# Performance work log

Measured on AMD Instinct MI355X. Metric: run time of the kernel, lower is better.

The kernel has to match this reference:

```python
import jax, jax.numpy as jnp
import numpy as np

EMBED_DIM = 768
NUM_HEADS = 12
HEAD_DIM = EMBED_DIM // NUM_HEADS


def setup_inputs() -> dict:
    key = jax.random.key(0)
    kx, kq, kk, kv, ko = jax.random.split(key, 5)
    B, S, D = 2, 2048, EMBED_DIM
    scale = 1.0 / np.sqrt(D)
    x = jax.random.normal(kx, (B, S, D), dtype=jnp.float32)
    # nn.Linear weight is [out, in]; y = x @ W.T. Store as [in, out] for y = x @ W.
    Wq = jax.random.normal(kq, (D, D), dtype=jnp.float32) * scale
    Wk = jax.random.normal(kk, (D, D), dtype=jnp.float32) * scale
    Wv = jax.random.normal(kv, (D, D), dtype=jnp.float32) * scale
    Wo = jax.random.normal(ko, (D, D), dtype=jnp.float32) * scale
    return {"x": x, "Wq": Wq, "Wk": Wk, "Wv": Wv, "Wo": Wo}


def reference(x, Wq, Wk, Wv, Wo):
    B, S, D = x.shape
    H, Hd = NUM_HEADS, HEAD_DIM
    # projections -> [B, H, S, Hd]
    q = (x @ Wq).reshape(B, S, H, Hd).transpose(0, 2, 1, 3)
    k = (x @ Wk).reshape(B, S, H, Hd).transpose(0, 2, 1, 3)
    v = (x @ Wv).reshape(B, S, H, Hd).transpose(0, 2, 1, 3)
    # scores [B, H, S, S], scaled by sqrt(head_dim)
    scores = jnp.einsum('bhqd,bhkd->bhqk', q, k) / jnp.sqrt(jnp.float32(Hd))
    attn = jax.nn.softmax(scores, axis=-1)
    out = jnp.einsum('bhqk,bhkd->bhqd', attn, v)  # [B, H, S, Hd]
    out = out.transpose(0, 2, 1, 3).reshape(B, S, D)
    return out @ Wo
```

## Files before the change

### kernel.cpp

```cpp
#include <hip/hip_runtime.h>
#include <hip/hip_bf16.h>
#include <cstdint>
#include <math.h>

#define DIM   768

typedef __bf16 bf16x8 __attribute__((ext_vector_type(8)));
typedef __bf16 bf16x2 __attribute__((ext_vector_type(2)));
typedef float f32x4 __attribute__((ext_vector_type(4)));
typedef unsigned short u16x8 __attribute__((ext_vector_type(8)));
typedef unsigned short u16x4 __attribute__((ext_vector_type(4)));

static __device__ __forceinline__ unsigned short f2bf(float f) {
  union { float f; unsigned u; } a; a.f = f;
  unsigned u = a.u;
  u += 0x7fffu + ((u >> 16) & 1u);
  return (unsigned short)(u >> 16);
}
static __device__ __forceinline__ unsigned pk2(float a, float b) {
  union { bf16x2 v; unsigned u; } x;
  x.v[0] = (__bf16)a; x.v[1] = (__bf16)b;
  return x.u;
}

static __device__ __forceinline__ f32x4 mfma16(bf16x8 a, bf16x8 b, f32x4 c) {
  return __builtin_amdgcn_mfma_f32_16x16x32_bf16(a, b, c, 0, 0, 0);
}

static __device__ __forceinline__ bf16x8 ld_bf8(const unsigned short* p) {
  return *reinterpret_cast<const bf16x8*>(p);
}

static __device__ __forceinline__ void gload_lds16(const void* g, void* l) {
  __builtin_amdgcn_global_load_lds(
      (const __attribute__((address_space(1))) void*)g,
      (__attribute__((address_space(3))) void*)l, 16, 0, 0);
}

#define EXP2 __builtin_amdgcn_exp2f

__global__ void k_cvt_x(const float* __restrict__ x, unsigned short* __restrict__ xb) {
  int i = (blockIdx.x * 256 + threadIdx.x) * 4;
  float4 v = *reinterpret_cast<const float4*>(x + i);
  u16x4 o;
  o[0] = f2bf(v.x); o[1] = f2bf(v.y); o[2] = f2bf(v.z); o[3] = f2bf(v.w);
  *reinterpret_cast<u16x4*>(xb + i) = o;
}

__global__ void k_tw(const float* __restrict__ Wq, const float* __restrict__ Wk,
                     const float* __restrict__ Wv, const float* __restrict__ Wo,
                     unsigned short* __restrict__ wqkvt, unsigned short* __restrict__ wot) {
  __shared__ unsigned short tile[64][68];
  const int wsel = blockIdx.z;
  const float* W = wsel == 0 ? Wq : wsel == 1 ? Wk : wsel == 2 ? Wv : Wo;
  const int n0 = blockIdx.x * 64, k0 = blockIdx.y * 64;
  const int t = threadIdx.x;
  const int kr = t >> 4, nc = (t & 15) * 4;
  for (int p = 0; p < 4; ++p) {
    int kk = kr + p * 16;
    float4 v = *reinterpret_cast<const float4*>(W + (size_t)(k0 + kk) * DIM + n0 + nc);
    tile[kk][nc]     = f2bf(v.x);
    tile[kk][nc + 1] = f2bf(v.y);
    tile[kk][nc + 2] = f2bf(v.z);
    tile[kk][nc + 3] = f2bf(v.w);
  }
  __syncthreads();
  const int nr = t >> 3, kc = (t & 7) * 8;
  for (int p = 0; p < 2; ++p) {
    int nn = nr + p * 32;
    u16x8 o;
    for (int j = 0; j < 8; ++j) o[j] = tile[kc + j][nn];
    unsigned short* dst = (wsel < 3)
        ? wqkvt + (size_t)(wsel * DIM + n0 + nn) * DIM + k0 + kc
        : wot + (size_t)(n0 + nn) * DIM + k0 + kc;
    *reinterpret_cast<u16x8*>(dst) = o;
  }
}

template <int EPI>
__global__ __launch_bounds__(256, 2) void k_gemm(
    const unsigned short* __restrict__ A, const unsigned short* __restrict__ Bt,
    unsigned short* __restrict__ qws, unsigned short* __restrict__ kws,
    unsigned short* __restrict__ vtws, float* __restrict__ out) {
  __shared__ alignas(16) unsigned short lA[128 * 64];
  __shared__ alignas(16) unsigned short lB[128 * 64];
  const int t = threadIdx.x;
  const int lane = t & 63, w = t >> 6;
  const int wr = w >> 1, wc = w & 1;
  const int r15 = lane & 15, rhi = lane >> 4;
  const int m0 = blockIdx.x * 128, n0 = blockIdx.y * 128;

  f32x4 acc[4][4] = {};

  for (int kt = 0; kt < 12; ++kt) {
    const int k0 = kt * 64;
    for (int i = 0; i < 4; ++i) {
      int f = i * 256 + t;
      int row = f >> 3;
      int cb = (f & 7) ^ (row & 7);
      gload_lds16(A + (size_t)(m0 + row) * DIM + k0 + cb * 8, (char*)lA + f * 16);
      gload_lds16(Bt + (size_t)(n0 + row) * DIM + k0 + cb * 8, (char*)lB + f * 16);
    }
    __syncthreads();
    for (int kk = 0; kk < 2; ++kk) {
      bf16x8 av[4], bv[4];
      for (int m = 0; m < 4; ++m) {
        int row = wr * 64 + m * 16 + r15;
        int cb = (kk * 4 + rhi) ^ (row & 7);
        av[m] = ld_bf8(lA + row * 64 + cb * 8);
      }
      for (int n = 0; n < 4; ++n) {
        int row = wc * 64 + n * 16 + r15;
        int cb = (kk * 4 + rhi) ^ (row & 7);
        bv[n] = ld_bf8(lB + row * 64 + cb * 8);
      }
      for (int m = 0; m < 4; ++m)
        for (int n = 0; n < 4; ++n)
          acc[m][n] = mfma16(av[m], bv[n], acc[m][n]);
    }
    __syncthreads();
  }

  for (int m = 0; m < 4; ++m) {
    for (int n = 0; n < 4; ++n) {
      for (int r = 0; r < 4; ++r) {
        int row = m0 + wr * 64 + m * 16 + rhi * 4 + r;
        int col = n0 + wc * 64 + n * 16 + r15;
        float v = acc[m][n][r];
        if (EPI == 0) {
          int wsel = col >= 1536 ? 2 : (col >= 768 ? 1 : 0);
          int c = col - wsel * 768;
          int h = c >> 6, d = c & 63;
          int b = row >> 11, s = row & 2047;
          size_t bh = (size_t)b * 12 + h;
          unsigned short bb = f2bf(v);
          if (wsel == 0)      qws[(bh * 2048 + s) * 64 + d] = bb;
          else if (wsel == 1) kws[(bh * 2048 + s) * 64 + d] = bb;
          else                vtws[(bh * 64 + d) * 2048 + s] = bb;
        } else {
          out[(size_t)row * DIM + col] = v;
        }
      }
    }
  }
}

__global__ __launch_bounds__(256) void k_attn(
    const unsigned short* __restrict__ qws, const unsigned short* __restrict__ kws,
    const unsigned short* __restrict__ vtws, unsigned short* __restrict__ ows) {
  __shared__ alignas(16) unsigned short lK[64 * 64];
  __shared__ alignas(16) unsigned short lV[64 * 64];
  __shared__ alignas(16) unsigned short lP[4][16 * 72];
  const int t = threadIdx.x;
  const int lane = t & 63, w = t >> 6;
  const int r15 = lane & 15, rhi = lane >> 4;
  const int bh = blockIdx.x;
  const int q0 = blockIdx.y * 64 + w * 16;
  const float SC = 0.18033688011112042f;

  const size_t qrow = ((size_t)bh * 2048 + q0 + r15) * 64;
  bf16x8 qa0 = ld_bf8(qws + qrow + rhi * 8);
  bf16x8 qa1 = ld_bf8(qws + qrow + 32 + rhi * 8);

  f32x4 oaccT[4] = {};
  float mrun = -INFINITY, lrun = 0.f;

  unsigned short* P = &lP[w][0];
  unsigned* Pw = (unsigned*)P;

  for (int kv = 0; kv < 2048; kv += 64) {
    for (int i = 0; i < 2; ++i) {
      int f = i * 256 + t;
      int row = f >> 3;
      int cb = (f & 7) ^ (row & 7);
      gload_lds16(kws + ((size_t)bh * 2048 + kv + row) * 64 + cb * 8, (char*)lK + f * 16);
      gload_lds16(vtws + ((size_t)bh * 64 + row) * 2048 + kv + cb * 8, (char*)lV + f * 16);
    }
    __syncthreads();

    f32x4 sT[4];
#pragma unroll
    for (int n = 0; n < 4; ++n) {
      int row = n * 16 + r15;
      bf16x8 b0 = ld_bf8(lK + row * 64 + ((rhi) ^ (row & 7)) * 8);
      bf16x8 b1 = ld_bf8(lK + row * 64 + ((4 + rhi) ^ (row & 7)) * 8);
      f32x4 z = {0.f, 0.f, 0.f, 0.f};
      z = mfma16(b0, qa0, z);
      z = mfma16(b1, qa1, z);
      sT[n] = z;
    }

    float mp = sT[0][0];
#pragma unroll
    for (int n = 0; n < 4; ++n)
      for (int r = 0; r < 4; ++r) mp = fmaxf(mp, sT[n][r]);
    mp = fmaxf(mp, __shfl_xor(mp, 16));
    mp = fmaxf(mp, __shfl_xor(mp, 32));
    float mps = mp * SC;

    if (!__all(mps <= mrun + 8.0f)) {
      float mn = fmaxf(mrun, mps);
      float fac = EXP2(mrun - mn);
      mrun = mn;
      lrun *= fac;
#pragma unroll
      for (int nd = 0; nd < 4; ++nd)
        for (int r = 0; r < 4; ++r) oaccT[nd][r] *= fac;
    }

    float p[4][4];
    float rs = 0.f;
#pragma unroll
    for (int n = 0; n < 4; ++n)
      for (int r = 0; r < 4; ++r) {
        p[n][r] = EXP2(fmaf(sT[n][r], SC, -mrun));
        rs += p[n][r];
      }
    rs += __shfl_xor(rs, 16);
    rs += __shfl_xor(rs, 32);
    lrun += rs;

#pragma unroll
    for (int n = 0; n < 4; ++n) {
      int kj = n * 16 + rhi * 4;
      Pw[r15 * 36 + (kj >> 1)]     = pk2(p[n][0], p[n][1]);
      Pw[r15 * 36 + (kj >> 1) + 1] = pk2(p[n][2], p[n][3]);
    }

    bf16x8 pa0 = ld_bf8(P + r15 * 72 + rhi * 8);
    bf16x8 pa1 = ld_bf8(P + r15 * 72 + 32 + rhi * 8);
#pragma unroll
    for (int nd = 0; nd < 4; ++nd) {
      int row = nd * 16 + r15;
      bf16x8 v0 = ld_bf8(lV + row * 64 + ((rhi) ^ (row & 7)) * 8);
      bf16x8 v1 = ld_bf8(lV + row * 64 + ((4 + rhi) ^ (row & 7)) * 8);
      oaccT[nd] = mfma16(v0, pa0, oaccT[nd]);
      oaccT[nd] = mfma16(v1, pa1, oaccT[nd]);
    }
    __syncthreads();
  }

  const int b = bh / 12, h = bh % 12;
  float inv = 1.0f / lrun;
  unsigned short* dst = ows + ((size_t)b * 2048 + q0 + r15) * DIM + h * 64;
#pragma unroll
  for (int nd = 0; nd < 4; ++nd) {
    int d = nd * 16 + rhi * 4;
    *(unsigned*)(dst + d)     = pk2(oaccT[nd][0] * inv, oaccT[nd][1] * inv);
    *(unsigned*)(dst + d + 2) = pk2(oaccT[nd][2] * inv, oaccT[nd][3] * inv);
  }
}

extern "C" void kernel_launch(void* const* d_in, const int* in_sizes, int n_in,
                              void* d_out, int out_size, void* d_ws, size_t ws_size,
                              hipStream_t stream) {
  (void)in_sizes; (void)n_in; (void)out_size;
  const float* x  = (const float*)d_in[0];
  const float* Wq = (const float*)d_in[1];
  const float* Wk = (const float*)d_in[2];
  const float* Wv = (const float*)d_in[3];
  const float* Wo = (const float*)d_in[4];
  float* out = (float*)d_out;

  char* ws = (char*)d_ws;
  unsigned short* xb    = (unsigned short*)(ws);
  unsigned short* wqkvt = (unsigned short*)(ws + 6291456);
  unsigned short* wot   = (unsigned short*)(ws + 9830400);
  unsigned short* qws   = (unsigned short*)(ws + 11010048);
  unsigned short* kws   = (unsigned short*)(ws + 17301504);
  unsigned short* vtws  = (unsigned short*)(ws + 23592960);
  unsigned short* ows   = (unsigned short*)(ws + 29884416);
  if (ws_size < 36175872u) return;

  k_cvt_x<<<3072, 256, 0, stream>>>(x, xb);
  k_tw<<<dim3(12, 12, 4), 256, 0, stream>>>(Wq, Wk, Wv, Wo, wqkvt, wot);
  k_gemm<0><<<dim3(32, 18), 256, 0, stream>>>(xb, wqkvt, qws, kws, vtws, nullptr);
  k_attn<<<dim3(24, 32), 256, 0, stream>>>(qws, kws, vtws, ows);
  k_gemm<1><<<dim3(32, 6), 256, 0, stream>>>(ows, wot, nullptr, nullptr, nullptr, out);
}
```

Before: 170.2 us.

## Double-buffer K/V tiles in attention kernel to overlap loads with compute

Splits the K and V LDS tiles into two buffers and issues the direct-to-LDS global loads for the next KV block before computing on the current one. One of the two barriers per iteration is dropped, and global load address calculation is hoisted out of the loop. The aim is to hide global memory latency behind the MFMA and softmax work. In exchange it doubles the K/V shared memory, which may lower occupancy, and it relies on the async loads having completed by the single barrier.

```diff
diff --git a/kernel.cpp b/kernel.cpp
--- a/kernel.cpp
+++ b/kernel.cpp
@@ -148,8 +148,8 @@
 __global__ __launch_bounds__(256) void k_attn(
     const unsigned short* __restrict__ qws, const unsigned short* __restrict__ kws,
     const unsigned short* __restrict__ vtws, unsigned short* __restrict__ ows) {
-  __shared__ alignas(16) unsigned short lK[64 * 64];
-  __shared__ alignas(16) unsigned short lV[64 * 64];
+  __shared__ alignas(16) unsigned short lK[2][64 * 64];
+  __shared__ alignas(16) unsigned short lV[2][64 * 64];
   __shared__ alignas(16) unsigned short lP[4][16 * 72];
   const int t = threadIdx.x;
   const int lane = t & 63, w = t >> 6;
@@ -158,6 +158,14 @@
   const int q0 = blockIdx.y * 64 + w * 16;
   const float SC = 0.18033688011112042f;
 
+  const int f0 = t, f1 = 256 + t;
+  const int row0 = f0 >> 3, row1 = f1 >> 3;
+  const int cb0 = (f0 & 7) ^ (row0 & 7), cb1 = (f1 & 7) ^ (row1 & 7);
+  const unsigned short* kg0 = kws + ((size_t)bh * 2048 + row0) * 64 + cb0 * 8;
+  const unsigned short* kg1 = kws + ((size_t)bh * 2048 + row1) * 64 + cb1 * 8;
+  const unsigned short* vg0 = vtws + ((size_t)bh * 64 + row0) * 2048 + cb0 * 8;
+  const unsigned short* vg1 = vtws + ((size_t)bh * 64 + row1) * 2048 + cb1 * 8;
+
   const size_t qrow = ((size_t)bh * 2048 + q0 + r15) * 64;
   bf16x8 qa0 = ld_bf8(qws + qrow + rhi * 8);
   bf16x8 qa1 = ld_bf8(qws + qrow + 32 + rhi * 8);
@@ -168,22 +176,29 @@
   unsigned short* P = &lP[w][0];
   unsigned* Pw = (unsigned*)P;
 
+#define STAGE(buf, kv) do { \
+    gload_lds16(kg0 + (size_t)(kv) * 64, (char*)lK[buf] + f0 * 16); \
+    gload_lds16(kg1 + (size_t)(kv) * 64, (char*)lK[buf] + f1 * 16); \
+    gload_lds16(vg0 + (kv),              (char*)lV[buf] + f0 * 16); \
+    gload_lds16(vg1 + (kv),              (char*)lV[buf] + f1 * 16); \
+  } while (0)
+
+  STAGE(0, 0);
+  __syncthreads();
+
+  int cur = 0;
   for (int kv = 0; kv < 2048; kv += 64) {
-    for (int i = 0; i < 2; ++i) {
-      int f = i * 256 + t;
-      int row = f >> 3;
-      int cb = (f & 7) ^ (row & 7);
-      gload_lds16(kws + ((size_t)bh * 2048 + kv + row) * 64 + cb * 8, (char*)lK + f * 16);
-      gload_lds16(vtws + ((size_t)bh * 64 + row) * 2048 + kv + cb * 8, (char*)lV + f * 16);
-    }
-    __syncthreads();
+    if (kv + 64 < 2048) STAGE(cur ^ 1, kv + 64);
+
+    const unsigned short* Kc = lK[cur];
+    const unsigned short* Vc = lV[cur];
 
     f32x4 sT[4];
 #pragma unroll
     for (int n = 0; n < 4; ++n) {
       int row = n * 16 + r15;
-      bf16x8 b0 = ld_bf8(lK + row * 64 + ((rhi) ^ (row & 7)) * 8);
-      bf16x8 b1 = ld_bf8(lK + row * 64 + ((4 + rhi) ^ (row & 7)) * 8);
+      bf16x8 b0 = ld_bf8(Kc + row * 64 + ((rhi) ^ (row & 7)) * 8);
+      bf16x8 b1 = ld_bf8(Kc + row * 64 + ((4 + rhi) ^ (row & 7)) * 8);
       f32x4 z = {0.f, 0.f, 0.f, 0.f};
       z = mfma16(b0, qa0, z);
       z = mfma16(b1, qa1, z);
@@ -232,13 +247,16 @@
 #pragma unroll
     for (int nd = 0; nd < 4; ++nd) {
       int row = nd * 16 + r15;
-      bf16x8 v0 = ld_bf8(lV + row * 64 + ((rhi) ^ (row & 7)) * 8);
-      bf16x8 v1 = ld_bf8(lV + row * 64 + ((4 + rhi) ^ (row & 7)) * 8);
+      bf16x8 v0 = ld_bf8(Vc + row * 64 + ((rhi) ^ (row & 7)) * 8);
+      bf16x8 v1 = ld_bf8(Vc + row * 64 + ((4 + rhi) ^ (row & 7)) * 8);
       oaccT[nd] = mfma16(v0, pa0, oaccT[nd]);
       oaccT[nd] = mfma16(v1, pa1, oaccT[nd]);
     }
+
     __syncthreads();
-  }
+    cur ^= 1;
+  }
+#undef STAGE
 
   const int b = bh / 12, h = bh % 12;
   float inv = 1.0f / lrun;
```

Result: no change. 171.1 us (+0.5%).
